# Optimization experiments

Hardware: AMD Instinct MI355X
Metric: run time of the kernel (lower is better)

The kernel has to match this reference:

```python
import jax, jax.numpy as jnp
import numpy as np

NEG_INF = -1e30


def setup_inputs() -> dict:
    key = jax.random.key(0)
    kq, kk, kv, ks = jax.random.split(key, 4)
    B, H, S, D = 2, 16, 2048, 64
    return {
        "q": jax.random.normal(kq, (B, H, S, D), dtype=jnp.float32),
        "k": jax.random.normal(kk, (B, H, S, D), dtype=jnp.float32),
        "v": jax.random.normal(kv, (B, H, S, D), dtype=jnp.float32),
        "sink_weights": jax.random.normal(ks, (H,), dtype=jnp.float32),
        "sliding_window": 1024,
    }


def reference(q, k, v, sink_weights, sliding_window):
    """Sliding-window causal attention with a learnable attention-sink logit.

    Equivalent to FlexAttention.forward with sink_weights given: an extra kv
    position (the sink) is appended whose score is replaced by sink_weights[h]
    and whose value is zero -> it only adds mass to the softmax denominator.
    """
    B, H, S_q, D = q.shape
    S_kv = k.shape[2]
    scale = 1.0 / np.sqrt(D)

    # [B, H, S_q, S_kv] raw scores
    scores = jnp.einsum("bhqd,bhkd->bhqk", q, k) * scale

    q_idx = jnp.arange(S_q)[:, None]
    kv_idx = jnp.arange(S_kv)[None, :]
    keep = (kv_idx <= q_idx) & (q_idx - kv_idx <= sliding_window)  # [S_q, S_kv]
    scores = jnp.where(keep[None, None], scores, NEG_INF)

    # sink column: per-head learnable logit, always visible
    sink_col = jnp.broadcast_to(
        sink_weights[None, :, None, None], (B, H, S_q, 1)
    )
    logits = jnp.concatenate([scores, sink_col], axis=-1)  # [B,H,S_q,S_kv+1]

    probs = jax.nn.softmax(logits, axis=-1)
    # sink value is zero, so only the first S_kv prob columns hit v
    out = jnp.einsum("bhqk,bhkd->bhqd", probs[..., :S_kv], v)
    return out
```

## Files before the change

### kernel.cpp

```cpp
#include <hip/hip_runtime.h>


typedef __bf16 bf16x8 __attribute__((ext_vector_type(8)));
typedef __bf16 bf16x4 __attribute__((ext_vector_type(4)));
typedef float  f32x16 __attribute__((ext_vector_type(16)));

#define NT 256
#define NEG_BIG (-3.0e38f)

__device__ __forceinline__ int swz(int row, int gran) {
    return row * 64 + ((gran ^ ((row >> 1) & 7)) << 3);
}

__device__ __forceinline__ bf16x4 xswap32(bf16x4 v) {
    union { bf16x4 v; int i[2]; } u;
    u.v = v;
    u.i[0] = __shfl_xor(u.i[0], 32, 64);
    u.i[1] = __shfl_xor(u.i[1], 32, 64);
    return u.v;
}

__device__ const int SEG_N[36]     = {2,1,1,2,1,1,1,1,1,2,1,1, 1,1,1,1,1,1,1,1,1,1,1,1,1,1,1,1,1,1,1,1,1,1,1,1};
__device__ const int SEG_IT[36][2] = {
  {0,1},{2,0},{3,0},{3,4},{4,0},{5,0},{5,0},{6,0},{6,0},{6,7},{7,0},{7,0},
  {8,0},{8,0},{8,0},{9,0},{9,0},{9,0},{10,0},{10,0},{10,0},{11,0},{11,0},{11,0},
  {12,0},{12,0},{12,0},{13,0},{13,0},{13,0},{14,0},{14,0},{14,0},{15,0},{15,0},{15,0}};
__device__ const int SEG_J0[36][2] = {
  {0,0},{0,0},{0,0},{6,0},{4,0},{0,0},{6,0},{0,0},{6,0},{12,0},{4,0},{10,0},
  {0,0},{6,0},{12,0},{0,0},{6,0},{12,0},{0,0},{6,0},{12,0},{0,0},{6,0},{12,0},
  {0,0},{6,0},{12,0},{0,0},{6,0},{12,0},{0,0},{6,0},{12,0},{0,0},{6,0},{12,0}};
__device__ const int SEG_J1[36][2] = {
  {2,4},{6,0},{6,0},{8,4},{10,0},{6,0},{12,0},{6,0},{12,0},{14,4},{10,0},{16,0},
  {6,0},{12,0},{18,0},{6,0},{12,0},{18,0},{6,0},{12,0},{18,0},{6,0},{12,0},{18,0},
  {6,0},{12,0},{18,0},{6,0},{12,0},{18,0},{6,0},{12,0},{18,0},{6,0},{12,0},{18,0}};
__device__ const int SEG_SX[36][2] = {
  {0,0},{0,0},{0,0},{1,0},{1,0},{0,0},{1,0},{0,0},{1,0},{2,0},{1,0},{2,0},
  {0,0},{1,0},{2,0},{0,0},{1,0},{2,0},{0,0},{1,0},{2,0},{0,0},{1,0},{2,0},
  {0,0},{1,0},{2,0},{0,0},{1,0},{2,0},{0,0},{1,0},{2,0},{0,0},{1,0},{2,0}};
__device__ const int NSEG_ITEM[16] = {1,1,1,2,2,2,3,3, 3,3,3,3,3,3,3,3};

__global__ __launch_bounds__(NT, 3) void flex_r10_main(
    const float* __restrict__ Q, const float* __restrict__ K,
    const float* __restrict__ V, const float* __restrict__ SINKW,
    const int* __restrict__ SWIN, void* __restrict__ WS,
    float* __restrict__ OUT, const int H, const int S)
{
    const int t    = threadIdx.x;
    const int lane = t & 63;
    const int w    = t >> 6;
    const int c    = lane & 31;
    const int hl   = lane >> 5;
    const int W    = SWIN[0];
    const float scale = 0.125f;

    const int NBH = gridDim.x / 36;
    const int bh  = blockIdx.x / 36;
    const int b36 = blockIdx.x - bh * 36;
    const int h   = bh % H;
    const float sw = SINKW[h];

    __shared__ __align__(16) __bf16 k_lds[2][64 * 64];
    __shared__ __align__(16) __bf16 v_lds[2][64 * 64];

    const size_t basebh = (size_t)bh * S * 64;
    const float4* kp4 = (const float4*)(K + basebh);
    const float4* vp4 = (const float4*)(V + basebh);
    __bf16* O_ws  = (__bf16*)WS;
    float2* ml_ws = (float2*)((char*)WS + (size_t)NBH * 48 * 16384);

    const int dgi = t & 15;
    const int kgi = t >> 4;
    float4 kreg[4], vreg[4];

    const int ns = SEG_N[b36];

    {
        const int it0 = SEG_IT[b36][0];
        const int ktA0 = (2 * it0 - 16 > 0) ? (2 * it0 - 16) : 0;
        const int kt = ktA0 + SEG_J0[b36][0];
        #pragma unroll
        for (int i = 0; i < 4; ++i) kreg[i] = kp4[kt * 1024 + i * NT + t];
        #pragma unroll
        for (int kk = 0; kk < 4; ++kk) vreg[kk] = vp4[kt * 1024 + (4 * kgi + kk) * 16 + dgi];
        #pragma unroll
        for (int i = 0; i < 4; ++i) {
            const int flat = i * NT + t;
            const int key = flat >> 4, dd = flat & 15;
            float4 f = kreg[i];
            bf16x4 b = { (__bf16)f.x, (__bf16)f.y, (__bf16)f.z, (__bf16)f.w };
            *(bf16x4*)&k_lds[0][swz(key, dd >> 1) + (dd & 1) * 4] = b;
        }
        {
            float4 a0 = vreg[0], a1 = vreg[1], a2 = vreg[2], a3 = vreg[3];
            bf16x4 w0 = { (__bf16)a0.x, (__bf16)a1.x, (__bf16)a2.x, (__bf16)a3.x };
            bf16x4 w1 = { (__bf16)a0.y, (__bf16)a1.y, (__bf16)a2.y, (__bf16)a3.y };
            bf16x4 w2 = { (__bf16)a0.z, (__bf16)a1.z, (__bf16)a2.z, (__bf16)a3.z };
            bf16x4 w3 = { (__bf16)a0.w, (__bf16)a1.w, (__bf16)a2.w, (__bf16)a3.w };
            const int gv = kgi >> 1, ov = (kgi & 1) * 4;
            *(bf16x4*)&v_lds[0][swz(4 * dgi + 0, gv) + ov] = w0;
            *(bf16x4*)&v_lds[0][swz(4 * dgi + 1, gv) + ov] = w1;
            *(bf16x4*)&v_lds[0][swz(4 * dgi + 2, gv) + ov] = w2;
            *(bf16x4*)&v_lds[0][swz(4 * dgi + 3, gv) + ov] = w3;
        }
    }

    int par = 0;

    for (int s = 0; s < ns; ++s) {
        const int item = SEG_IT[b36][s];
        const int j0   = SEG_J0[b36][s];
        const int j1   = SEG_J1[b36][s];
        const int sidx = SEG_SX[b36][s];
        const int ktA  = (2 * item - 16 > 0) ? (2 * item - 16) : 0;
        const int qw0  = item * 128 + 32 * w;
        const int qi   = qw0 + c;

        bf16x8 bq[4];
        {
            const float4* qp4 = (const float4*)(Q + basebh + (size_t)qi * 64);
            #pragma unroll
            for (int ks = 0; ks < 4; ++ks) {
                float4 f0 = qp4[4 * ks + 2 * hl];
                float4 f1 = qp4[4 * ks + 2 * hl + 1];
                bq[ks][0] = (__bf16)(f0.x * scale); bq[ks][1] = (__bf16)(f0.y * scale);
                bq[ks][2] = (__bf16)(f0.z * scale); bq[ks][3] = (__bf16)(f0.w * scale);
                bq[ks][4] = (__bf16)(f1.x * scale); bq[ks][5] = (__bf16)(f1.y * scale);
                bq[ks][6] = (__bf16)(f1.z * scale); bq[ks][7] = (__bf16)(f1.w * scale);
            }
        }

        float mrun = (sidx == 0) ? sw : NEG_BIG;
        float lrun = (sidx == 0) ? 1.0f : 0.0f;
        f32x16 accO0, accO1;
        #pragma unroll
        for (int i = 0; i < 16; ++i) { accO0[i] = 0.0f; accO1[i] = 0.0f; }

        for (int j = j0; j < j1; ++j) {
            const int k0 = (ktA + j) * 64;

            __syncthreads();

            int nkt = -1;
            if (j + 1 < j1) nkt = ktA + j + 1;
            else if (s + 1 < ns) {
                const int it2 = SEG_IT[b36][s + 1];
                const int ktA2 = (2 * it2 - 16 > 0) ? (2 * it2 - 16) : 0;
                nkt = ktA2 + SEG_J0[b36][s + 1];
            }
            if (nkt >= 0) {
                #pragma unroll
                for (int i = 0; i < 4; ++i) kreg[i] = kp4[nkt * 1024 + i * NT + t];
                #pragma unroll
                for (int kk = 0; kk < 4; ++kk) vreg[kk] = vp4[nkt * 1024 + (4 * kgi + kk) * 16 + dgi];
            }

            const __bf16* kb = k_lds[par];
            const __bf16* vb = v_lds[par];
            f32x16 accS0, accS1;
            #pragma unroll
            for (int i = 0; i < 16; ++i) { accS0[i] = 0.0f; accS1[i] = 0.0f; }
            #pragma unroll
            for (int ks = 0; ks < 4; ++ks) {
                bf16x8 ka0 = *(const bf16x8*)&kb[swz(c,      2 * ks + hl)];
                bf16x8 ka1 = *(const bf16x8*)&kb[swz(32 + c, 2 * ks + hl)];
                accS0 = __builtin_amdgcn_mfma_f32_32x32x16_bf16(ka0, bq[ks], accS0, 0, 0, 0);
                accS1 = __builtin_amdgcn_mfma_f32_32x32x16_bf16(ka1, bq[ks], accS1, 0, 0, 0);
            }

            const bool interior = (k0 + 63 <= qw0) && (qw0 + 31 - k0 <= W);
            if (!interior) {
                #pragma unroll
                for (int rg = 0; rg < 16; ++rg) {
                    const int kb2 = (rg & 3) + 8 * (rg >> 2) + 4 * hl;
                    const int ki0 = k0 + kb2, ki1 = k0 + 32 + kb2;
                    if (!((ki0 <= qi) && (qi - ki0 <= W))) accS0[rg] = -1e30f;
                    if (!((ki1 <= qi) && (qi - ki1 <= W))) accS1[rg] = -1e30f;
                }
            }

            float mx = accS0[0];
            #pragma unroll
            for (int i = 1; i < 16; ++i) mx = fmaxf(mx, accS0[i]);
            #pragma unroll
            for (int i = 0; i < 16; ++i) mx = fmaxf(mx, accS1[i]);
            mx = fmaxf(mx, __shfl_xor(mx, 32, 64));
            const float mnew  = fmaxf(mrun, mx);
            const float alpha = __expf(mrun - mnew);
            float ps = 0.0f;
            #pragma unroll
            for (int i = 0; i < 16; ++i) { float p = __expf(accS0[i] - mnew); accS0[i] = p; ps += p; }
            #pragma unroll
            for (int i = 0; i < 16; ++i) { float p = __expf(accS1[i] - mnew); accS1[i] = p; ps += p; }
            ps += __shfl_xor(ps, 32, 64);
            lrun = lrun * alpha + ps;
            mrun = mnew;
            #pragma unroll
            for (int i = 0; i < 16; ++i) { accO0[i] *= alpha; accO1[i] *= alpha; }

            bf16x4 qA = { (__bf16)accS0[0],  (__bf16)accS0[1],  (__bf16)accS0[2],  (__bf16)accS0[3]  };
            bf16x4 qB = { (__bf16)accS0[4],  (__bf16)accS0[5],  (__bf16)accS0[6],  (__bf16)accS0[7]  };
            bf16x4 qC = { (__bf16)accS0[8],  (__bf16)accS0[9],  (__bf16)accS0[10], (__bf16)accS0[11] };
            bf16x4 qD = { (__bf16)accS0[12], (__bf16)accS0[13], (__bf16)accS0[14], (__bf16)accS0[15] };
            bf16x4 qE = { (__bf16)accS1[0],  (__bf16)accS1[1],  (__bf16)accS1[2],  (__bf16)accS1[3]  };
            bf16x4 qF = { (__bf16)accS1[4],  (__bf16)accS1[5],  (__bf16)accS1[6],  (__bf16)accS1[7]  };
            bf16x4 qG = { (__bf16)accS1[8],  (__bf16)accS1[9],  (__bf16)accS1[10], (__bf16)accS1[11] };
            bf16x4 qH = { (__bf16)accS1[12], (__bf16)accS1[13], (__bf16)accS1[14], (__bf16)accS1[15] };
            bf16x4 r0 = xswap32(hl ? qA : qB);
            bf16x4 r1 = xswap32(hl ? qC : qD);
            bf16x4 r2 = xswap32(hl ? qE : qF);
            bf16x4 r3 = xswap32(hl ? qG : qH);
            bf16x4 lo0 = hl ? r0 : qA, hi0 = hl ? qB : r0;
            bf16x4 lo1 = hl ? r1 : qC, hi1 = hl ? qD : r1;
            bf16x4 lo2 = hl ? r2 : qE, hi2 = hl ? qF : r2;
            bf16x4 lo3 = hl ? r3 : qG, hi3 = hl ? qH : r3;
            bf16x8 bp[4];
            #pragma unroll
            for (int e = 0; e < 4; ++e) {
                bp[0][e] = lo0[e]; bp[0][4+e] = hi0[e];
                bp[1][e] = lo1[e]; bp[1][4+e] = hi1[e];
                bp[2][e] = lo2[e]; bp[2][4+e] = hi2[e];
                bp[3][e] = lo3[e]; bp[3][4+e] = hi3[e];
            }

            #pragma unroll
            for (int ks = 0; ks < 4; ++ks) {
                bf16x8 va0 = *(const bf16x8*)&vb[swz(c,      2 * ks + hl)];
                bf16x8 va1 = *(const bf16x8*)&vb[swz(32 + c, 2 * ks + hl)];
                accO0 = __builtin_amdgcn_mfma_f32_32x32x16_bf16(va0, bp[ks], accO0, 0, 0, 0);
                accO1 = __builtin_amdgcn_mfma_f32_32x32x16_bf16(va1, bp[ks], accO1, 0, 0, 0);
            }

            if (nkt >= 0) {
                const int np = par ^ 1;
                #pragma unroll
                for (int i = 0; i < 4; ++i) {
                    const int flat = i * NT + t;
                    const int key = flat >> 4, dd = flat & 15;
                    float4 f = kreg[i];
                    bf16x4 b = { (__bf16)f.x, (__bf16)f.y, (__bf16)f.z, (__bf16)f.w };
                    *(bf16x4*)&k_lds[np][swz(key, dd >> 1) + (dd & 1) * 4] = b;
                }
                float4 a0 = vreg[0], a1 = vreg[1], a2 = vreg[2], a3 = vreg[3];
                bf16x4 w0 = { (__bf16)a0.x, (__bf16)a1.x, (__bf16)a2.x, (__bf16)a3.x };
                bf16x4 w1 = { (__bf16)a0.y, (__bf16)a1.y, (__bf16)a2.y, (__bf16)a3.y };
                bf16x4 w2 = { (__bf16)a0.z, (__bf16)a1.z, (__bf16)a2.z, (__bf16)a3.z };
                bf16x4 w3 = { (__bf16)a0.w, (__bf16)a1.w, (__bf16)a2.w, (__bf16)a3.w };
                const int gv = kgi >> 1, ov = (kgi & 1) * 4;
                *(bf16x4*)&v_lds[np][swz(4 * dgi + 0, gv) + ov] = w0;
                *(bf16x4*)&v_lds[np][swz(4 * dgi + 1, gv) + ov] = w1;
                *(bf16x4*)&v_lds[np][swz(4 * dgi + 2, gv) + ov] = w2;
                *(bf16x4*)&v_lds[np][swz(4 * dgi + 3, gv) + ov] = w3;
            }
            par ^= 1;
        }

        if (item < 3) {
            const float inv = 1.0f / lrun;
            float* ob = OUT + basebh + (size_t)qi * 64;
            #pragma unroll
            for (int rg = 0; rg < 4; ++rg) {
                float4 f0 = { accO0[4*rg+0]*inv, accO0[4*rg+1]*inv,
                              accO0[4*rg+2]*inv, accO0[4*rg+3]*inv };
                float4 f1 = { accO1[4*rg+0]*inv, accO1[4*rg+1]*inv,
                              accO1[4*rg+2]*inv, accO1[4*rg+3]*inv };
                *(float4*)&ob[     8 * rg + 4 * hl] = f0;
                *(float4*)&ob[32 + 8 * rg + 4 * hl] = f1;
            }
        } else {
            const int slot = (bh * 16 + item) * 3 + sidx;
            const int qrel = 32 * w + c;
            if (hl == 0) ml_ws[(size_t)slot * 128 + qrel] = make_float2(mrun, lrun);
            __bf16* Os = O_ws + (size_t)slot * 8192 + (size_t)qrel * 64;
            #pragma unroll
            for (int qd = 0; qd < 4; ++qd) {
                const int d0 = 8 * qd + 4 * hl;
                bf16x4 b0 = { (__bf16)accO0[4*qd+0], (__bf16)accO0[4*qd+1],
                              (__bf16)accO0[4*qd+2], (__bf16)accO0[4*qd+3] };
                bf16x4 b1 = { (__bf16)accO1[4*qd+0], (__bf16)accO1[4*qd+1],
                              (__bf16)accO1[4*qd+2], (__bf16)accO1[4*qd+3] };
                *(bf16x4*)&Os[d0]      = b0;
                *(bf16x4*)&Os[32 + d0] = b1;
            }
        }
    }
}

__global__ __launch_bounds__(256) void flex_r10_combine(
    const void* __restrict__ WS, float* __restrict__ OUT, const int H, const int S)
{
    const int NBH  = gridDim.x / 13;
    const int bi   = blockIdx.x;
    const int bh   = bi / 13;
    const int item = 3 + (bi - bh * 13);
    const int ns   = NSEG_ITEM[item];
    const int t    = threadIdx.x;
    const int q    = t >> 1;
    const int half = t & 1;

    const __bf16* O_ws = (const __bf16*)WS;
    const float2* ml_ws = (const float2*)((const char*)WS + (size_t)NBH * 48 * 16384);
    const int base = (bh * 16 + item) * 3;

    float m[3], lv[3], a[3];
    float mst = NEG_BIG;
    for (int s = 0; s < ns; ++s) {
        float2 e = ml_ws[(size_t)(base + s) * 128 + q];
        m[s] = e.x; lv[s] = e.y;
        mst = fmaxf(mst, m[s]);
    }
    float lst = 0.0f;
    for (int s = 0; s < ns; ++s) { a[s] = __expf(m[s] - mst); lst += a[s] * lv[s]; }
    const float inv = 1.0f / lst;

    float acc[32];
    #pragma unroll
    for (int i = 0; i < 32; ++i) acc[i] = 0.0f;
    for (int s = 0; s < ns; ++s) {
        const __bf16* Os = O_ws + (size_t)(base + s) * 8192 + (size_t)q * 64 + 32 * half;
        const float as = a[s];
        #pragma unroll
        for (int v8 = 0; v8 < 4; ++v8) {
            bf16x8 o = *(const bf16x8*)&Os[8 * v8];
            #pragma unroll
            for (int jj = 0; jj < 8; ++jj) acc[8 * v8 + jj] += as * (float)o[jj];
        }
    }

    float* dst = OUT + (size_t)bh * S * 64 + (size_t)(item * 128 + q) * 64 + 32 * half;
    #pragma unroll
    for (int v4 = 0; v4 < 8; ++v4) {
        float4 f = { acc[4*v4+0] * inv, acc[4*v4+1] * inv,
                     acc[4*v4+2] * inv, acc[4*v4+3] * inv };
        *(float4*)&dst[4 * v4] = f;
    }
}

extern "C" void kernel_launch(void* const* d_in, const int* in_sizes, int n_in,
                              void* d_out, int out_size, void* d_ws, size_t ws_size,
                              hipStream_t stream) {
    const float* q     = (const float*)d_in[0];
    const float* k     = (const float*)d_in[1];
    const float* v     = (const float*)d_in[2];
    const float* sinkw = (const float*)d_in[3];
    const int*   swin  = (const int*)d_in[4];
    float* out = (float*)d_out;

    const int H = in_sizes[3];
    const int S = 2048;
    const int B = in_sizes[0] / (H * S * 64);
    const int NBH = B * H;

    flex_r10_main<<<dim3(NBH * 36), NT, 0, stream>>>(q, k, v, sinkw, swin, d_ws, out, H, S);
    flex_r10_combine<<<dim3(NBH * 13), 256, 0, stream>>>(d_ws, out, H, S);
}
```

Before: 142.3 us.

## Pre-convert K/V to bf16 and stream tiles via global_load_lds DMA

Adds a pre-pass kernel that converts K to bf16 and V to a transposed bf16 layout in the workspace. The main kernel then fills its double-buffered LDS tiles with direct global-to-LDS loads, replacing the register staging and in-loop fp32-to-bf16 conversion. Softmax moves to base-2 exponentials by folding log2(e) into the Q scale and sink logit, and the max and sum reductions become trees. Occupancy hint rises to 4 waves, at the cost of an extra kernel launch and a round trip of K/V through global memory.

```diff
diff --git a/kernel.cpp b/kernel.cpp
--- a/kernel.cpp
+++ b/kernel.cpp
@@ -7,6 +7,7 @@
 
 #define NT 256
 #define NEG_BIG (-3.0e38f)
+#define LOG2E 1.44269504089f
 
 __device__ __forceinline__ int swz(int row, int gran) {
     return row * 64 + ((gran ^ ((row >> 1) & 7)) << 3);
@@ -19,6 +20,10 @@
     u.i[1] = __shfl_xor(u.i[1], 32, 64);
     return u.v;
 }
+
+#define GLDS(gp, lp) __builtin_amdgcn_global_load_lds( \
+    (const __attribute__((address_space(1))) unsigned int*)(gp), \
+    (__attribute__((address_space(3))) unsigned int*)(lp), 16, 0, 0)
 
 __device__ const int SEG_N[36]     = {2,1,1,2,1,1,1,1,1,2,1,1, 1,1,1,1,1,1,1,1,1,1,1,1,1,1,1,1,1,1,1,1,1,1,1,1};
 __device__ const int SEG_IT[36][2] = {
@@ -39,9 +44,49 @@
   {0,0},{1,0},{2,0},{0,0},{1,0},{2,0},{0,0},{1,0},{2,0},{0,0},{1,0},{2,0}};
 __device__ const int NSEG_ITEM[16] = {1,1,1,2,2,2,3,3, 3,3,3,3,3,3,3,3};
 
-__global__ __launch_bounds__(NT, 3) void flex_r10_main(
-    const float* __restrict__ Q, const float* __restrict__ K,
-    const float* __restrict__ V, const float* __restrict__ SINKW,
+__global__ __launch_bounds__(256) void flex_r12_pre(
+    const float* __restrict__ K, const float* __restrict__ V,
+    void* __restrict__ WS, const int S)
+{
+    const int t    = threadIdx.x;
+    const int nkt  = S >> 6;
+    const int NBH  = gridDim.x / nkt;
+    const int bh   = blockIdx.x / nkt;
+    const int kt   = blockIdx.x - bh * nkt;
+    const size_t basebh = (size_t)bh * S * 64;
+
+    __bf16* Kb = (__bf16*)WS + basebh;
+    __bf16* Vt = (__bf16*)WS + (size_t)NBH * S * 64 + basebh;
+
+    const float4* kp4 = (const float4*)(K + basebh + (size_t)kt * 64 * 64);
+    const float4* vp4 = (const float4*)(V + basebh + (size_t)kt * 64 * 64);
+
+    #pragma unroll
+    for (int i = 0; i < 4; ++i) {
+        const int f = i * 256 + t;
+        const int key = f >> 4, d4 = f & 15;
+        float4 x = kp4[f];
+        bf16x4 b = { (__bf16)x.x, (__bf16)x.y, (__bf16)x.z, (__bf16)x.w };
+        *(bf16x4*)&Kb[(size_t)(kt * 64 + key) * 64 + d4 * 4] = b;
+    }
+    const int dgi = t & 15, kgi = t >> 4;
+    float4 a0 = vp4[(4 * kgi + 0) * 16 + dgi];
+    float4 a1 = vp4[(4 * kgi + 1) * 16 + dgi];
+    float4 a2 = vp4[(4 * kgi + 2) * 16 + dgi];
+    float4 a3 = vp4[(4 * kgi + 3) * 16 + dgi];
+    bf16x4 w0 = { (__bf16)a0.x, (__bf16)a1.x, (__bf16)a2.x, (__bf16)a3.x };
+    bf16x4 w1 = { (__bf16)a0.y, (__bf16)a1.y, (__bf16)a2.y, (__bf16)a3.y };
+    bf16x4 w2 = { (__bf16)a0.z, (__bf16)a1.z, (__bf16)a2.z, (__bf16)a3.z };
+    bf16x4 w3 = { (__bf16)a0.w, (__bf16)a1.w, (__bf16)a2.w, (__bf16)a3.w };
+    const int kb0 = kt * 64 + 4 * kgi;
+    *(bf16x4*)&Vt[(size_t)(4 * dgi + 0) * S + kb0] = w0;
+    *(bf16x4*)&Vt[(size_t)(4 * dgi + 1) * S + kb0] = w1;
+    *(bf16x4*)&Vt[(size_t)(4 * dgi + 2) * S + kb0] = w2;
+    *(bf16x4*)&Vt[(size_t)(4 * dgi + 3) * S + kb0] = w3;
+}
+
+__global__ __launch_bounds__(NT, 4) void flex_r12_main(
+    const float* __restrict__ Q, const float* __restrict__ SINKW,
     const int* __restrict__ SWIN, void* __restrict__ WS,
     float* __restrict__ OUT, const int H, const int S)
 {
@@ -51,57 +96,49 @@
     const int c    = lane & 31;
     const int hl   = lane >> 5;
     const int W    = SWIN[0];
-    const float scale = 0.125f;
+    const float qscale = 0.125f * LOG2E;
 
     const int NBH = gridDim.x / 36;
     const int bh  = blockIdx.x / 36;
     const int b36 = blockIdx.x - bh * 36;
     const int h   = bh % H;
-    const float sw = SINKW[h];
+    const float sw = SINKW[h] * LOG2E;
 
     __shared__ __align__(16) __bf16 k_lds[2][64 * 64];
     __shared__ __align__(16) __bf16 v_lds[2][64 * 64];
 
     const size_t basebh = (size_t)bh * S * 64;
-    const float4* kp4 = (const float4*)(K + basebh);
-    const float4* vp4 = (const float4*)(V + basebh);
-    __bf16* O_ws  = (__bf16*)WS;
-    float2* ml_ws = (float2*)((char*)WS + (size_t)NBH * 48 * 16384);
-
-    const int dgi = t & 15;
-    const int kgi = t >> 4;
-    float4 kreg[4], vreg[4];
+    const char* KbB = (const char*)WS + basebh * 2;
+    const char* VtB = (const char*)WS + (size_t)NBH * S * 128 + basebh * 2;
+    __bf16* O_ws  = (__bf16*)WS + (size_t)2 * NBH * S * 64;
+    float2* ml_ws = (float2*)((char*)WS + (size_t)4 * NBH * S * 64
+                                        + (size_t)NBH * 48 * 16384);
+
+    int koff[2], voff[2];
+    #pragma unroll
+    for (int i = 0; i < 2; ++i) {
+        const int qc  = 2 * w + i;
+        const int row = qc * 8 + (lane >> 3);
+        const int gr  = (lane & 7) ^ ((row >> 1) & 7);
+        koff[i] = row * 128 + gr * 16;
+        voff[i] = row * (S * 2) + gr * 16;
+    }
+
+    auto dma = [&](int kt, int buf) {
+        const char* ks = KbB + (size_t)kt * 8192;
+        const char* vs = VtB + (size_t)kt * 128;
+        #pragma unroll
+        for (int i = 0; i < 2; ++i) {
+            GLDS(ks + koff[i], (char*)&k_lds[buf][0] + (2 * w + i) * 1024);
+            GLDS(vs + voff[i], (char*)&v_lds[buf][0] + (2 * w + i) * 1024);
+        }
+    };
 
     const int ns = SEG_N[b36];
-
     {
         const int it0 = SEG_IT[b36][0];
         const int ktA0 = (2 * it0 - 16 > 0) ? (2 * it0 - 16) : 0;
-        const int kt = ktA0 + SEG_J0[b36][0];
-        #pragma unroll
-        for (int i = 0; i < 4; ++i) kreg[i] = kp4[kt * 1024 + i * NT + t];
-        #pragma unroll
-        for (int kk = 0; kk < 4; ++kk) vreg[kk] = vp4[kt * 1024 + (4 * kgi + kk) * 16 + dgi];
-        #pragma unroll
-        for (int i = 0; i < 4; ++i) {
-            const int flat = i * NT + t;
-            const int key = flat >> 4, dd = flat & 15;
-            float4 f = kreg[i];
-            bf16x4 b = { (__bf16)f.x, (__bf16)f.y, (__bf16)f.z, (__bf16)f.w };
-            *(bf16x4*)&k_lds[0][swz(key, dd >> 1) + (dd & 1) * 4] = b;
-        }
-        {
-            float4 a0 = vreg[0], a1 = vreg[1], a2 = vreg[2], a3 = vreg[3];
-            bf16x4 w0 = { (__bf16)a0.x, (__bf16)a1.x, (__bf16)a2.x, (__bf16)a3.x };
-            bf16x4 w1 = { (__bf16)a0.y, (__bf16)a1.y, (__bf16)a2.y, (__bf16)a3.y };
-            bf16x4 w2 = { (__bf16)a0.z, (__bf16)a1.z, (__bf16)a2.z, (__bf16)a3.z };
-            bf16x4 w3 = { (__bf16)a0.w, (__bf16)a1.w, (__bf16)a2.w, (__bf16)a3.w };
-            const int gv = kgi >> 1, ov = (kgi & 1) * 4;
-            *(bf16x4*)&v_lds[0][swz(4 * dgi + 0, gv) + ov] = w0;
-            *(bf16x4*)&v_lds[0][swz(4 * dgi + 1, gv) + ov] = w1;
-            *(bf16x4*)&v_lds[0][swz(4 * dgi + 2, gv) + ov] = w2;
-            *(bf16x4*)&v_lds[0][swz(4 * dgi + 3, gv) + ov] = w3;
-        }
+        dma(ktA0 + SEG_J0[b36][0], 0);
     }
 
     int par = 0;
@@ -122,10 +159,10 @@
             for (int ks = 0; ks < 4; ++ks) {
                 float4 f0 = qp4[4 * ks + 2 * hl];
                 float4 f1 = qp4[4 * ks + 2 * hl + 1];
-                bq[ks][0] = (__bf16)(f0.x * scale); bq[ks][1] = (__bf16)(f0.y * scale);
-                bq[ks][2] = (__bf16)(f0.z * scale); bq[ks][3] = (__bf16)(f0.w * scale);
-                bq[ks][4] = (__bf16)(f1.x * scale); bq[ks][5] = (__bf16)(f1.y * scale);
-                bq[ks][6] = (__bf16)(f1.z * scale); bq[ks][7] = (__bf16)(f1.w * scale);
+                bq[ks][0] = (__bf16)(f0.x * qscale); bq[ks][1] = (__bf16)(f0.y * qscale);
+                bq[ks][2] = (__bf16)(f0.z * qscale); bq[ks][3] = (__bf16)(f0.w * qscale);
+                bq[ks][4] = (__bf16)(f1.x * qscale); bq[ks][5] = (__bf16)(f1.y * qscale);
+                bq[ks][6] = (__bf16)(f1.z * qscale); bq[ks][7] = (__bf16)(f1.w * qscale);
             }
         }
 
@@ -147,12 +184,7 @@
                 const int ktA2 = (2 * it2 - 16 > 0) ? (2 * it2 - 16) : 0;
                 nkt = ktA2 + SEG_J0[b36][s + 1];
             }
-            if (nkt >= 0) {
-                #pragma unroll
-                for (int i = 0; i < 4; ++i) kreg[i] = kp4[nkt * 1024 + i * NT + t];
-                #pragma unroll
-                for (int kk = 0; kk < 4; ++kk) vreg[kk] = vp4[nkt * 1024 + (4 * kgi + kk) * 16 + dgi];
-            }
+            if (nkt >= 0) dma(nkt, par ^ 1);
 
             const __bf16* kb = k_lds[par];
             const __bf16* vb = v_lds[par];
@@ -178,19 +210,26 @@
                 }
             }
 
-            float mx = accS0[0];
-            #pragma unroll
-            for (int i = 1; i < 16; ++i) mx = fmaxf(mx, accS0[i]);
-            #pragma unroll
-            for (int i = 0; i < 16; ++i) mx = fmaxf(mx, accS1[i]);
+            float mm[8];
+            #pragma unroll
+            for (int i = 0; i < 8; ++i)
+                mm[i] = fmaxf(fmaxf(accS0[2*i], accS0[2*i+1]),
+                              fmaxf(accS1[2*i], accS1[2*i+1]));
+            float mx = fmaxf(fmaxf(fmaxf(mm[0], mm[1]), fmaxf(mm[2], mm[3])),
+                             fmaxf(fmaxf(mm[4], mm[5]), fmaxf(mm[6], mm[7])));
             mx = fmaxf(mx, __shfl_xor(mx, 32, 64));
             const float mnew  = fmaxf(mrun, mx);
-            const float alpha = __expf(mrun - mnew);
-            float ps = 0.0f;
-            #pragma unroll
-            for (int i = 0; i < 16; ++i) { float p = __expf(accS0[i] - mnew); accS0[i] = p; ps += p; }
-            #pragma unroll
-            for (int i = 0; i < 16; ++i) { float p = __expf(accS1[i] - mnew); accS1[i] = p; ps += p; }
+            const float alpha = exp2f(mrun - mnew);
+            #pragma unroll
+            for (int i = 0; i < 16; ++i) accS0[i] = exp2f(accS0[i] - mnew);
+            #pragma unroll
+            for (int i = 0; i < 16; ++i) accS1[i] = exp2f(accS1[i] - mnew);
+            float pp[8];
+            #pragma unroll
+            for (int i = 0; i < 8; ++i)
+                pp[i] = (accS0[2*i] + accS0[2*i+1]) + (accS1[2*i] + accS1[2*i+1]);
+            float ps = ((pp[0] + pp[1]) + (pp[2] + pp[3]))
+                     + ((pp[4] + pp[5]) + (pp[6] + pp[7]));
             ps += __shfl_xor(ps, 32, 64);
             lrun = lrun * alpha + ps;
             mrun = mnew;
@@ -230,27 +269,6 @@
                 accO1 = __builtin_amdgcn_mfma_f32_32x32x16_bf16(va1, bp[ks], accO1, 0, 0, 0);
             }
 
-            if (nkt >= 0) {
-                const int np = par ^ 1;
-                #pragma unroll
-                for (int i = 0; i < 4; ++i) {
-                    const int flat = i * NT + t;
-                    const int key = flat >> 4, dd = flat & 15;
-                    float4 f = kreg[i];
-                    bf16x4 b = { (__bf16)f.x, (__bf16)f.y, (__bf16)f.z, (__bf16)f.w };
-                    *(bf16x4*)&k_lds[np][swz(key, dd >> 1) + (dd & 1) * 4] = b;
-                }
-                float4 a0 = vreg[0], a1 = vreg[1], a2 = vreg[2], a3 = vreg[3];
-                bf16x4 w0 = { (__bf16)a0.x, (__bf16)a1.x, (__bf16)a2.x, (__bf16)a3.x };
-                bf16x4 w1 = { (__bf16)a0.y, (__bf16)a1.y, (__bf16)a2.y, (__bf16)a3.y };
-                bf16x4 w2 = { (__bf16)a0.z, (__bf16)a1.z, (__bf16)a2.z, (__bf16)a3.z };
-                bf16x4 w3 = { (__bf16)a0.w, (__bf16)a1.w, (__bf16)a2.w, (__bf16)a3.w };
-                const int gv = kgi >> 1, ov = (kgi & 1) * 4;
-                *(bf16x4*)&v_lds[np][swz(4 * dgi + 0, gv) + ov] = w0;
-                *(bf16x4*)&v_lds[np][swz(4 * dgi + 1, gv) + ov] = w1;
-                *(bf16x4*)&v_lds[np][swz(4 * dgi + 2, gv) + ov] = w2;
-                *(bf16x4*)&v_lds[np][swz(4 * dgi + 3, gv) + ov] = w3;
-            }
             par ^= 1;
         }
 
@@ -285,7 +303,7 @@
     }
 }
 
-__global__ __launch_bounds__(256) void flex_r10_combine(
+__global__ __launch_bounds__(256) void flex_r12_combine(
     const void* __restrict__ WS, float* __restrict__ OUT, const int H, const int S)
 {
     const int NBH  = gridDim.x / 13;
@@ -297,8 +315,9 @@
     const int q    = t >> 1;
     const int half = t & 1;
 
-    const __bf16* O_ws = (const __bf16*)WS;
-    const float2* ml_ws = (const float2*)((const char*)WS + (size_t)NBH * 48 * 16384);
+    const __bf16* O_ws = (const __bf16*)WS + (size_t)2 * NBH * S * 64;
+    const float2* ml_ws = (const float2*)((const char*)WS + (size_t)4 * NBH * S * 64
+                                          + (size_t)NBH * 48 * 16384);
     const int base = (bh * 16 + item) * 3;
 
     float m[3], lv[3], a[3];
@@ -309,7 +328,7 @@
         mst = fmaxf(mst, m[s]);
     }
     float lst = 0.0f;
-    for (int s = 0; s < ns; ++s) { a[s] = __expf(m[s] - mst); lst += a[s] * lv[s]; }
+    for (int s = 0; s < ns; ++s) { a[s] = exp2f(m[s] - mst); lst += a[s] * lv[s]; }
     const float inv = 1.0f / lst;
 
     float acc[32];
@@ -350,6 +369,7 @@
     const int B = in_sizes[0] / (H * S * 64);
     const int NBH = B * H;
 
-    flex_r10_main<<<dim3(NBH * 36), NT, 0, stream>>>(q, k, v, sinkw, swin, d_ws, out, H, S);
-    flex_r10_combine<<<dim3(NBH * 13), 256, 0, stream>>>(d_ws, out, H, S);
-}
+    flex_r12_pre    <<<dim3(NBH * (S / 64)), 256, 0, stream>>>(k, v, d_ws, S);
+    flex_r12_main   <<<dim3(NBH * 36),       NT,  0, stream>>>(q, sinkw, swin, d_ws, out, H, S);
+    flex_r12_combine<<<dim3(NBH * 13),       256, 0, stream>>>(d_ws, out, H, S);
+}
```

Measured after the change: 149.2 us. 4.9% more time.
